# Optimization experiments

Hardware: AMD Instinct MI355X
Metric: run time of the kernel (lower is better)

Reference implementation:

```python
import jax, jax.numpy as jnp
import numpy as np

E = 2_000_000   # edges
N = 200_000     # atoms
B = 100         # bond types (10 species, ordered pairs)
R = 13          # reduced_matrix_element (SK integrals per bond)
G = 512         # num_xgrid
T = 10          # atom types
OE = 4          # n_onsite_Es
R_MIN, R_MAX = 1.0, 6.0  # SK table distance range (Bohr-ish)


def setup_inputs() -> dict:
    key = jax.random.key(0)
    k1, k2, k3, k4, k5, k6 = jax.random.split(key, 6)
    rij = jax.random.uniform(k1, (E,), jnp.float32, 1.5, 5.5)
    edge_type = jax.random.randint(k2, (E,), 0, B, jnp.int32)
    atom_type = jax.random.randint(k3, (N,), 0, T, jnp.int32)
    xx = jnp.linspace(R_MIN, R_MAX, G, dtype=jnp.float32)  # sorted distance grid
    hopping_param = jax.random.normal(k4, (B, R, G), jnp.float32)
    overlap_param = jax.random.normal(k5, (B, R, G), jnp.float32)
    onsite_param = jax.random.normal(k6, (T, OE, 1), jnp.float32)
    return {"rij": rij, "edge_type": edge_type, "atom_type": atom_type,
            "xx": xx, "hopping_param": hopping_param,
            "overlap_param": overlap_param, "onsite_param": onsite_param}


def _interp_by_type(rij, edge_type, xx, table):
    """Fused gather + linear interpolation, keyed by edge_type.

    Replaces the original per-bond-type masked loop: for each edge, pick the
    [R, G] SK table for its bond type and linearly interpolate along the
    distance grid at rij. Returns [E, R].
    """
    g = xx.shape[0]
    # interval index for each edge (clamped -> linear extrapolation at edges)
    idx = jnp.clip(jnp.searchsorted(xx, rij, side="right") - 1, 0, g - 2)  # [E]
    x0 = xx[idx]
    x1 = xx[idx + 1]
    t = ((rij - x0) / (x1 - x0))[:, None]  # [E, 1]
    # advanced indexing on axes 0 and 2, full slice on axis 1 -> [E, R]
    y0 = table[edge_type, :, idx]
    y1 = table[edge_type, :, idx + 1]
    return y0 * (1.0 - t) + y1 * t


def reference(rij, edge_type, atom_type, xx, hopping_param, overlap_param, onsite_param):
    edge_features = _interp_by_type(rij, edge_type, xx, hopping_param)   # [E, R]
    edge_overlap = _interp_by_type(rij, edge_type, xx, overlap_param)    # [E, R]
    # dftb onsite: direct per-atom-type parameter lookup (num_paras == 1)
    node_features = onsite_param[atom_type, :, 0]                         # [N, OE]
    return edge_features, edge_overlap, node_features
```

## Files before the change

kernel.cpp:

```cpp
#include <hip/hip_runtime.h>

#define E_CNT 2000000
#define N_CNT 200000
#define B_CNT 100
#define R_CNT 13
#define G_CNT 512
#define T_CNT 10
#define OE_CNT 4

#define P2_ROW 32
#define P2_FLOATS ((size_t)B_CNT * G_CNT * P2_ROW)
#define P2_BYTES (P2_FLOATS * 4)

#define EDGES_PER_BLOCK 64
#define EDGE_BLOCKS (E_CNT / EDGES_PER_BLOCK)
#define NODE_BLOCKS ((N_CNT + 255) / 256)
#define OUT_OVL_OFF ((size_t)E_CNT * R_CNT)
#define OUT_NODE_OFF ((size_t)2 * E_CNT * R_CNT)

#define SH_STRIDE 20

typedef float v4f __attribute__((ext_vector_type(4)));

__global__ __launch_bounds__(256) void repack_interleave_kernel(
    const float* __restrict__ hopping,
    const float* __restrict__ overlap,
    float* __restrict__ P2)
{
    int tid = blockIdx.x * 256 + threadIdx.x;
    int b = tid >> 9;
    int g = tid & (G_CNT - 1);
    float h[16], o[16];
    #pragma unroll
    for (int r = 0; r < R_CNT; ++r) {
        size_t src = (((size_t)b * R_CNT + r) << 9) + g;
        h[r] = hopping[src];
        o[r] = overlap[src];
    }
    h[13] = h[14] = h[15] = 0.0f;
    o[13] = o[14] = o[15] = 0.0f;
    float* dst = P2 + (size_t)tid * P2_ROW;
    #pragma unroll
    for (int q = 0; q < 4; ++q) {
        v4f hv = { h[4*q], h[4*q+1], h[4*q+2], h[4*q+3] };
        v4f ov = { o[4*q], o[4*q+1], o[4*q+2], o[4*q+3] };
        *(v4f*)(dst + 4 * q)      = hv;
        *(v4f*)(dst + 16 + 4 * q) = ov;
    }
}

__global__ __launch_bounds__(256) void fused_kernel(
    const float* __restrict__ rij,
    const int*   __restrict__ edge_type,
    const float* __restrict__ P2,
    const int*   __restrict__ atom_type,
    const float* __restrict__ onsite,
    float* __restrict__ out)
{
    if (blockIdx.x < EDGE_BLOCKS) {
        __shared__ float shh[EDGES_PER_BLOCK * SH_STRIDE];
        __shared__ float sho[EDGES_PER_BLOCK * SH_STRIDE];

        int tid = threadIdx.x;
        int eL = tid >> 2;
        int j  = tid & 3;
        int e  = blockIdx.x * EDGES_PER_BLOCK + eL;

        float r = __builtin_nontemporal_load(rij + e);
        int   b = __builtin_nontemporal_load(edge_type + e);

        const float inv_dx = 511.0f / 5.0f;
        float s = (r - 1.0f) * inv_dx;
        int idx = (int)s;
        idx = max(0, min(G_CNT - 2, idx));
        float t = s - (float)idx;
        float omt = 1.0f - t;

        const float* row = P2 + ((size_t)((b << 9) + idx)) * P2_ROW + 4 * j;
        v4f h0 = *(const v4f*)(row);
        v4f h1 = *(const v4f*)(row + P2_ROW);
        v4f o0 = *(const v4f*)(row + 16);
        v4f o1 = *(const v4f*)(row + 16 + P2_ROW);

        v4f vh = h0 * omt + h1 * t;
        v4f vo = o0 * omt + o1 * t;

        *(v4f*)(shh + eL * SH_STRIDE + 4 * j) = vh;
        *(v4f*)(sho + eL * SH_STRIDE + 4 * j) = vo;
        __syncthreads();

        if (tid < 208) {
            unsigned f0 = (unsigned)tid * 4u;
            float ph[4], po[4];
            #pragma unroll
            for (int k = 0; k < 4; ++k) {
                unsigned f = f0 + k;
                unsigned ee = f / 13u;
                unsigned rr = f - ee * 13u;
                ph[k] = shh[ee * SH_STRIDE + rr];
                po[k] = sho[ee * SH_STRIDE + rr];
            }
            v4f qh = { ph[0], ph[1], ph[2], ph[3] };
            v4f qo = { po[0], po[1], po[2], po[3] };
            size_t ob = (size_t)blockIdx.x * (EDGES_PER_BLOCK * R_CNT) + f0;
            __builtin_nontemporal_store(qh, (v4f*)(out + ob));
            __builtin_nontemporal_store(qo, (v4f*)(out + OUT_OVL_OFF + ob));
        }
    } else {
        int n = (blockIdx.x - EDGE_BLOCKS) * 256 + threadIdx.x;
        if (n < N_CNT) {
            int t = atom_type[n];
            v4f v = { onsite[t * OE_CNT + 0],
                      onsite[t * OE_CNT + 1],
                      onsite[t * OE_CNT + 2],
                      onsite[t * OE_CNT + 3] };
            __builtin_nontemporal_store(v, (v4f*)(out + OUT_NODE_OFF + (size_t)n * OE_CNT));
        }
    }
}

__global__ __launch_bounds__(256) void dftbsk_fallback(
    const float* __restrict__ rij,
    const int*   __restrict__ edge_type,
    const int*   __restrict__ atom_type,
    const float* __restrict__ xx,
    const float* __restrict__ hopping,
    const float* __restrict__ overlap,
    const float* __restrict__ onsite,
    float*       __restrict__ out)
{
    __shared__ float sxx[G_CNT];
    for (int i = threadIdx.x; i < G_CNT; i += blockDim.x) sxx[i] = xx[i];
    __syncthreads();

    long long gid = (long long)blockIdx.x * blockDim.x + threadIdx.x;
    if (gid < E_CNT) {
        int e = (int)gid;
        float r = rij[e];
        int b = edge_type[e];
        const float inv_dx = (float)(G_CNT - 1) / 5.0f;
        int idx = (int)floorf((r - 1.0f) * inv_dx);
        idx = max(0, min(G_CNT - 2, idx));
        while (idx > 0 && r < sxx[idx]) --idx;
        while (idx < G_CNT - 2 && r >= sxx[idx + 1]) ++idx;
        float x0 = sxx[idx], x1 = sxx[idx + 1];
        float t = (r - x0) / (x1 - x0);
        float omt = 1.0f - t;
        const float* hb = hopping + (size_t)b * (R_CNT * G_CNT) + idx;
        const float* ob = overlap + (size_t)b * (R_CNT * G_CNT) + idx;
        float* outh = out + (size_t)e * R_CNT;
        float* outo = out + OUT_OVL_OFF + (size_t)e * R_CNT;
        #pragma unroll
        for (int rr = 0; rr < R_CNT; ++rr)
            outh[rr] = hb[rr * G_CNT] * omt + hb[rr * G_CNT + 1] * t;
        #pragma unroll
        for (int rr = 0; rr < R_CNT; ++rr)
            outo[rr] = ob[rr * G_CNT] * omt + ob[rr * G_CNT + 1] * t;
    } else if (gid < (long long)E_CNT + N_CNT) {
        int n = (int)(gid - E_CNT);
        int t = atom_type[n];
        float4 v;
        v.x = onsite[t * OE_CNT + 0];
        v.y = onsite[t * OE_CNT + 1];
        v.z = onsite[t * OE_CNT + 2];
        v.w = onsite[t * OE_CNT + 3];
        *(float4*)(out + OUT_NODE_OFF + (size_t)n * OE_CNT) = v;
    }
}

extern "C" void kernel_launch(void* const* d_in, const int* in_sizes, int n_in,
                              void* d_out, int out_size, void* d_ws, size_t ws_size,
                              hipStream_t stream) {
    const float* rij        = (const float*)d_in[0];
    const int*   edge_type  = (const int*)d_in[1];
    const int*   atom_type  = (const int*)d_in[2];
    const float* xx         = (const float*)d_in[3];
    const float* hopping    = (const float*)d_in[4];
    const float* overlap    = (const float*)d_in[5];
    const float* onsite     = (const float*)d_in[6];
    float* out = (float*)d_out;

    if (ws_size >= P2_BYTES) {
        float* P2 = (float*)d_ws;
        repack_interleave_kernel<<<(B_CNT * G_CNT) / 256, 256, 0, stream>>>(
            hopping, overlap, P2);
        fused_kernel<<<EDGE_BLOCKS + NODE_BLOCKS, 256, 0, stream>>>(
            rij, edge_type, P2, atom_type, onsite, out);
    } else {
        const long long total = (long long)E_CNT + N_CNT;
        const int grid = (int)((total + 255) / 256);
        dftbsk_fallback<<<grid, 256, 0, stream>>>(rij, edge_type, atom_type, xx,
                                                  hopping, overlap, onsite, out);
    }
}
```

Baseline: 265.9 us.

## Split hopping/overlap tables and route each to separate XCD groups for L2 locality

Stores the hopping and overlap tables as separate 16-float-row arrays instead of one interleaved 32-float row. Each edge chunk is now handled by two blocks, one per table, and blocks are assigned by blockIdx modulo 8. This relies on round-robin XCD dispatch, so XCDs 0-3 only touch the hopping table and XCDs 4-7 only the overlap table. Each XCD's L2 then caches half the table footprint (about 3.3MB instead of 6.5MB). The cost is that rij and edge_type are read twice and the per-edge index math is repeated in twice as many blocks.

Measured after the change: 281.9 us. 1.06x slower.

```diff
diff --git a/kernel.cpp b/kernel.cpp
--- a/kernel.cpp
+++ b/kernel.cpp
@@ -8,12 +8,14 @@
 #define T_CNT 10
 #define OE_CNT 4
 
-#define P2_ROW 32
-#define P2_FLOATS ((size_t)B_CNT * G_CNT * P2_ROW)
-#define P2_BYTES (P2_FLOATS * 4)
+#define P_ROW 16
+#define P_ONE ((size_t)B_CNT * G_CNT * P_ROW)
+#define P_BYTES_TOTAL (2 * P_ONE * 4)
 
 #define EDGES_PER_BLOCK 64
-#define EDGE_BLOCKS (E_CNT / EDGES_PER_BLOCK)
+#define EDGE_CHUNKS (E_CNT / EDGES_PER_BLOCK)
+#define SLOTS ((EDGE_CHUNKS + 3) / 4)
+#define EDGE_BLOCKS (SLOTS * 8)
 #define NODE_BLOCKS ((N_CNT + 255) / 256)
 #define OUT_OVL_OFF ((size_t)E_CNT * R_CNT)
 #define OUT_NODE_OFF ((size_t)2 * E_CNT * R_CNT)
@@ -22,10 +24,11 @@
 
 typedef float v4f __attribute__((ext_vector_type(4)));
 
-__global__ __launch_bounds__(256) void repack_interleave_kernel(
+__global__ __launch_bounds__(256) void repack2_kernel(
     const float* __restrict__ hopping,
     const float* __restrict__ overlap,
-    float* __restrict__ P2)
+    float* __restrict__ Ph,
+    float* __restrict__ Po)
 {
     int tid = blockIdx.x * 256 + threadIdx.x;
     int b = tid >> 9;
@@ -39,35 +42,46 @@
     }
     h[13] = h[14] = h[15] = 0.0f;
     o[13] = o[14] = o[15] = 0.0f;
-    float* dst = P2 + (size_t)tid * P2_ROW;
+    float* dh = Ph + (size_t)tid * P_ROW;
+    float* doo = Po + (size_t)tid * P_ROW;
     #pragma unroll
     for (int q = 0; q < 4; ++q) {
         v4f hv = { h[4*q], h[4*q+1], h[4*q+2], h[4*q+3] };
         v4f ov = { o[4*q], o[4*q+1], o[4*q+2], o[4*q+3] };
-        *(v4f*)(dst + 4 * q)      = hv;
-        *(v4f*)(dst + 16 + 4 * q) = ov;
-    }
-}
-
-__global__ __launch_bounds__(256) void fused_kernel(
+        *(v4f*)(dh + 4 * q)  = hv;
+        *(v4f*)(doo + 4 * q) = ov;
+    }
+}
+
+__global__ __launch_bounds__(256) void sk_kernel(
     const float* __restrict__ rij,
     const int*   __restrict__ edge_type,
-    const float* __restrict__ P2,
+    const float* __restrict__ Ph,
+    const float* __restrict__ Po,
     const int*   __restrict__ atom_type,
     const float* __restrict__ onsite,
     float* __restrict__ out)
 {
-    if (blockIdx.x < EDGE_BLOCKS) {
-        __shared__ float shh[EDGES_PER_BLOCK * SH_STRIDE];
-        __shared__ float sho[EDGES_PER_BLOCK * SH_STRIDE];
+    unsigned bid = blockIdx.x;
+    if (bid < EDGE_BLOCKS) {
+        unsigned xcd  = bid & 7u;
+        unsigned slot = bid >> 3;
+        bool is_o = xcd >= 4u;
+        unsigned chunk = slot * 4u + (xcd & 3u);
+        if (chunk >= EDGE_CHUNKS) return;
+
+        const float* T = is_o ? Po : Ph;
+        float* obase = out + (is_o ? OUT_OVL_OFF : (size_t)0);
+
+        __shared__ float sh[EDGES_PER_BLOCK * SH_STRIDE];
 
         int tid = threadIdx.x;
         int eL = tid >> 2;
         int j  = tid & 3;
-        int e  = blockIdx.x * EDGES_PER_BLOCK + eL;
+        int e  = (int)chunk * EDGES_PER_BLOCK + eL;
 
         float r = __builtin_nontemporal_load(rij + e);
-        int   b = __builtin_nontemporal_load(edge_type + e);
+        int b = __builtin_nontemporal_load(edge_type + e);
 
         const float inv_dx = 511.0f / 5.0f;
         float s = (r - 1.0f) * inv_dx;
@@ -76,38 +90,30 @@
         float t = s - (float)idx;
         float omt = 1.0f - t;
 
-        const float* row = P2 + ((size_t)((b << 9) + idx)) * P2_ROW + 4 * j;
-        v4f h0 = *(const v4f*)(row);
-        v4f h1 = *(const v4f*)(row + P2_ROW);
-        v4f o0 = *(const v4f*)(row + 16);
-        v4f o1 = *(const v4f*)(row + 16 + P2_ROW);
-
-        v4f vh = h0 * omt + h1 * t;
-        v4f vo = o0 * omt + o1 * t;
-
-        *(v4f*)(shh + eL * SH_STRIDE + 4 * j) = vh;
-        *(v4f*)(sho + eL * SH_STRIDE + 4 * j) = vo;
+        size_t base = ((size_t)((b << 9) + idx)) * P_ROW + 4 * j;
+        v4f y0 = *(const v4f*)(T + base);
+        v4f y1 = *(const v4f*)(T + base + P_ROW);
+        v4f v = y0 * omt + y1 * t;
+
+        *(v4f*)(sh + eL * SH_STRIDE + 4 * j) = v;
         __syncthreads();
 
         if (tid < 208) {
             unsigned f0 = (unsigned)tid * 4u;
-            float ph[4], po[4];
+            float q[4];
             #pragma unroll
             for (int k = 0; k < 4; ++k) {
                 unsigned f = f0 + k;
                 unsigned ee = f / 13u;
                 unsigned rr = f - ee * 13u;
-                ph[k] = shh[ee * SH_STRIDE + rr];
-                po[k] = sho[ee * SH_STRIDE + rr];
+                q[k] = sh[ee * SH_STRIDE + rr];
             }
-            v4f qh = { ph[0], ph[1], ph[2], ph[3] };
-            v4f qo = { po[0], po[1], po[2], po[3] };
-            size_t ob = (size_t)blockIdx.x * (EDGES_PER_BLOCK * R_CNT) + f0;
-            __builtin_nontemporal_store(qh, (v4f*)(out + ob));
-            __builtin_nontemporal_store(qo, (v4f*)(out + OUT_OVL_OFF + ob));
+            v4f qv = { q[0], q[1], q[2], q[3] };
+            size_t ob = (size_t)chunk * (EDGES_PER_BLOCK * R_CNT) + f0;
+            __builtin_nontemporal_store(qv, (v4f*)(obase + ob));
         }
     } else {
-        int n = (blockIdx.x - EDGE_BLOCKS) * 256 + threadIdx.x;
+        int n = (int)(bid - EDGE_BLOCKS) * 256 + threadIdx.x;
         if (n < N_CNT) {
             int t = atom_type[n];
             v4f v = { onsite[t * OE_CNT + 0],
@@ -180,12 +186,13 @@
     const float* onsite     = (const float*)d_in[6];
     float* out = (float*)d_out;
 
-    if (ws_size >= P2_BYTES) {
-        float* P2 = (float*)d_ws;
-        repack_interleave_kernel<<<(B_CNT * G_CNT) / 256, 256, 0, stream>>>(
-            hopping, overlap, P2);
-        fused_kernel<<<EDGE_BLOCKS + NODE_BLOCKS, 256, 0, stream>>>(
-            rij, edge_type, P2, atom_type, onsite, out);
+    if (ws_size >= P_BYTES_TOTAL) {
+        float* Ph = (float*)d_ws;
+        float* Po = Ph + P_ONE;
+        repack2_kernel<<<(B_CNT * G_CNT) / 256, 256, 0, stream>>>(
+            hopping, overlap, Ph, Po);
+        sk_kernel<<<EDGE_BLOCKS + NODE_BLOCKS, 256, 0, stream>>>(
+            rij, edge_type, Ph, Po, atom_type, onsite, out);
     } else {
         const long long total = (long long)E_CNT + N_CNT;
         const int grid = (int)((total + 255) / 256);
```
